# Kernel optimization log

Measured on AMD Instinct MI355X. Metric: run time of the kernel, lower is better.

The kernel has to match this reference:

```python
import jax, jax.numpy as jnp
import numpy as np
from jax import lax

N, C, A, K, D = 2, 256, 3, 20, 256  # batch, channels, anchors, topk person cells, rn_fc_dim
BOX = 4
SIZES = [(80, 128), (40, 64), (20, 32), (10, 16)]
DN = ('NCHW', 'OIHW', 'NCHW')


def _conv(x, w, b):
    return lax.conv_general_dilated(x, w, (1, 1), 'SAME', dimension_numbers=DN) + b[None, :, None, None]


def setup_inputs() -> dict:
    key = jax.random.key(0)
    ks = iter(jax.random.split(key, 40))
    d = {}
    for i, (h, w) in enumerate(SIZES):
        d['feat%d' % i] = jax.random.normal(next(ks), (N, C, h, w), jnp.float32)
    def wfn(shape, s=0.05):
        return jax.random.normal(next(ks), shape, jnp.float32) * s
    d['pc1_w'] = wfn((C, C, 3, 3)); d['pc1_b'] = jnp.zeros((C,), jnp.float32)
    d['pc2_w'] = wfn((C, C, 3, 3)); d['pc2_b'] = jnp.zeros((C,), jnp.float32)
    d['oc1_w'] = wfn((C, C, 3, 3)); d['oc1_b'] = jnp.zeros((C,), jnp.float32)
    d['oc2_w'] = wfn((C, C, 3, 3)); d['oc2_b'] = jnp.zeros((C,), jnp.float32)
    # relation-net FCs: first takes concat(object, person) -> 2C in
    d['rn1_w'] = wfn((D, 2 * C)); d['rn1_b'] = jnp.zeros((D,), jnp.float32)
    d['rn2_w'] = wfn((D, D)); d['rn2_b'] = jnp.zeros((D,), jnp.float32)
    # heads
    d['pl_w'] = wfn((A, C, 1, 1), 0.01); d['pl_b'] = jnp.zeros((A,), jnp.float32)
    d['pd_w'] = wfn((A * BOX, C, 1, 1), 0.01); d['pd_b'] = jnp.zeros((A * BOX,), jnp.float32)
    d['ol_w'] = wfn((A, D), 0.01); d['ol_b'] = jnp.zeros((A,), jnp.float32)
    d['od_w'] = wfn((A * BOX, C, 1, 1), 0.01); d['od_b'] = jnp.zeros((A * BOX,), jnp.float32)
    return d


def _find_top_cells(hidden, logits, topk):
    hid_l, sc_l = [], []
    for h_map, lg in zip(hidden, logits):
        n, c, H, W = h_map.shape
        cell_scores = jnp.max(lg, axis=1).reshape(n, -1)          # (N, HW)
        ts, tc = lax.top_k(cell_scores, topk)                      # (N, K)
        hv = h_map.reshape(n, c, -1)                               # (N, C, HW)
        hid_l.append(jnp.take_along_axis(hv, tc[:, None, :], axis=2))  # (N, C, K)
        sc_l.append(ts)
    scores = jnp.concatenate(sc_l, axis=1)                         # (N, L*K)
    hid = jnp.concatenate(hid_l, axis=2)                           # (N, C, L*K)
    _, keep = lax.top_k(scores, topk)
    return jnp.take_along_axis(hid, keep[:, None, :], axis=2)      # (N, C, K)


def _forward(feats, pc1_w, pc1_b, pc2_w, pc2_b, oc1_w, oc1_b, oc2_w, oc2_b,
             rn1_w, rn1_b, rn2_w, rn2_b, pl_w, pl_b, pd_w, pd_b, ol_w, ol_b, od_w, od_b):
    # person branch
    p_hid, p_log, p_del = [], [], []
    for x in feats:
        x = jax.nn.relu(_conv(x, pc1_w, pc1_b))
        x = jax.nn.relu(_conv(x, pc2_w, pc2_b))
        p_hid.append(x)
        p_log.append(_conv(x, pl_w, pl_b))
        p_del.append(_conv(x, pd_w, pd_b))
    topk_person = _find_top_cells(p_hid, p_log, K)                 # (N, C, K)
    pf = topk_person.transpose(0, 2, 1)                            # (N, K, C)
    # object branch: fc1(concat(o, p)) == o @ Wo.T + p @ Wp.T + b (concat order: object first)
    Wo, Wp = rn1_w[:, :C], rn1_w[:, C:]
    p_proj = jnp.einsum('nkc,dc->nkd', pf, Wp) + rn1_b             # (N, K, D)
    o_log, o_del = [], []
    for x in feats:
        n, _, H, W = x.shape
        y = jax.nn.relu(_conv(x, oc1_w, oc1_b))
        y = jax.nn.relu(_conv(y, oc2_w, oc2_b))
        o_del.append(_conv(y, od_w, od_b))
        yf = y.reshape(n, C, H * W).transpose(0, 2, 1)             # (N, HW, C)
        o_proj = jnp.einsum('nsc,dc->nsd', yf, Wo)                 # (N, HW, D)
        h = jax.nn.relu(o_proj[:, :, None, :] + p_proj[:, None, :, :])  # (N, HW, K, D)
        h = h.sum(axis=2)                                          # (N, HW, D)
        h = jax.nn.relu(jnp.einsum('nsd,ed->nse', h, rn2_w) + rn2_b)
        ol = jnp.einsum('nsd,ad->nsa', h, ol_w) + ol_b             # (N, HW, A)
        o_log.append(ol.transpose(0, 2, 1).reshape(n, A, H, W))
    return tuple(p_log) + tuple(p_del) + tuple(o_log) + tuple(o_del)


def reference(feat0, feat1, feat2, feat3, pc1_w, pc1_b, pc2_w, pc2_b, oc1_w, oc1_b, oc2_w, oc2_b,
              rn1_w, rn1_b, rn2_w, rn2_b, pl_w, pl_b, pd_w, pd_b, ol_w, ol_b, od_w, od_b):
    return _forward([feat0, feat1, feat2, feat3], pc1_w, pc1_b, pc2_w, pc2_b, oc1_w, oc1_b,
                    oc2_w, oc2_b, rn1_w, rn1_b, rn2_w, rn2_b, pl_w, pl_b, pd_w, pd_b,
                    ol_w, ol_b, od_w, od_b)
```

## Files before the change

### kernel.cpp

```cpp
#include <hip/hip_runtime.h>
#include <cstdint>
#include <cstddef>

typedef __bf16 bf16x8 __attribute__((ext_vector_type(8)));
typedef float  f32x16 __attribute__((ext_vector_type(16)));

union U16 { bf16x8 v; uint4 q; };
union U8  { __bf16 h[4]; unsigned long long u; };

typedef __attribute__((address_space(1))) const unsigned char gas_t;
typedef __attribute__((address_space(3))) unsigned char las_t;
__device__ __forceinline__ void async16(const void* g, void* l) {
    __builtin_amdgcn_global_load_lds((gas_t*)g, (las_t*)l, 16, 0, 0);
}

__device__ __forceinline__ int lvl256(int bx) {
    return (bx < 40) ? 0 : (bx < 50) ? 1 : (bx < 53) ? 2 : 3;
}
__device__ __forceinline__ int tbase256(int lv) {
    return (lv == 0) ? 0 : (lv == 1) ? 40 : (lv == 2) ? 50 : 53;
}
__device__ __forceinline__ size_t loffE(int lv) {
    return (lv == 0) ? 0 : (lv == 1) ? 5242880 : (lv == 2) ? 6553600 : 6881280;
}
__device__ __forceinline__ size_t plog_off(int lv) {
    return (lv == 0) ? 0 : (lv == 1) ? 61440 : (lv == 2) ? 76800 : 80640;
}
__device__ __forceinline__ size_t pdel_off(int lv) {
    return (lv == 0) ? 81600 : (lv == 1) ? 327360 : (lv == 2) ? 388800 : 404160;
}
__device__ __forceinline__ size_t olog_off(int lv) {
    return (lv == 0) ? 408000 : (lv == 1) ? 469440 : (lv == 2) ? 484800 : 488640;
}
__device__ __forceinline__ size_t odel_off(int lv) {
    return (lv == 0) ? 489600 : (lv == 1) ? 735360 : (lv == 2) ? 796800 : 812160;
}
__device__ __forceinline__ int soff_l(int lv) {
    return (lv == 0) ? 0 : (lv == 1) ? 20480 : (lv == 2) ? 25600 : 26880;
}

__global__ __launch_bounds__(256) void prep_all_k(
    const float* f0, const float* f1, const float* f2, const float* f3,
    const float* pc1w, const float* pc2w, const float* oc1w, const float* oc2w,
    const float* __restrict__ rn1w, const float* __restrict__ rn2w,
    __bf16* __restrict__ wtap, float* __restrict__ WpT,
    __bf16* __restrict__ Wo16, __bf16* __restrict__ rn216,
    unsigned* __restrict__ zrow32, __bf16* __restrict__ x16)
{
    int bid = blockIdx.x, tid = threadIdx.x;
    if (bid < 576) {
        int which = bid / 144, r = bid - which * 144, t = r >> 4, c16 = r & 15;
        const float* src = (which == 0) ? pc1w : (which == 1) ? pc2w
                         : (which == 2) ? oc1w : oc2w;
        __bf16* dst = wtap + (size_t)which * 589824;
        int co = tid;
        U16 a, b;
#pragma unroll
        for (int j = 0; j < 8; ++j)
            a.v[j] = (__bf16)src[(size_t)(co * 256 + c16 * 16 + j) * 9 + t];
#pragma unroll
        for (int j = 0; j < 8; ++j)
            b.v[j] = (__bf16)src[(size_t)(co * 256 + c16 * 16 + 8 + j) * 9 + t];
        size_t o = ((size_t)((t * 16 + c16) * 256 + co)) << 4;
        *(uint4*)&dst[o] = a.q;
        *(uint4*)&dst[o + 8] = b.q;
    } else if (bid < 832) {
        int d = bid - 576, c = tid;
        WpT[c * 256 + d] = rn1w[(size_t)d * 512 + 256 + c];
        Wo16[((c >> 4) * 256 + d) * 16 + (c & 15)] = (__bf16)rn1w[(size_t)d * 512 + c];
        rn216[((c >> 4) * 256 + d) * 16 + (c & 15)] = (__bf16)rn2w[(size_t)d * 256 + c];
        if (d == 0) zrow32[c] = 0u;
    } else {
        int u = bid - 832;
        int bx = u >> 5, rr = u & 31, n = rr >> 4, ch = rr & 15;
        int lv = lvl256(bx);
        int HW = 10240 >> (2 * lv);
        int p = (bx - tbase256(lv)) * 256 + tid;
        if (p >= HW) return;
        const float* f = (lv == 0) ? f0 : (lv == 1) ? f1 : (lv == 2) ? f2 : f3;
        const float* src = f + (size_t)n * 256 * HW + (size_t)ch * 16 * HW + p;
        U16 a, b;
#pragma unroll
        for (int j = 0; j < 8; ++j) a.v[j] = (__bf16)src[(size_t)j * HW];
#pragma unroll
        for (int j = 0; j < 8; ++j) b.v[j] = (__bf16)src[(size_t)(8 + j) * HW];
        size_t o = loffE(lv) + (size_t)n * HW * 256 + (((size_t)ch * HW + p) << 4);
        *(uint4*)&x16[o] = a.q;
        *(uint4*)&x16[o + 8] = b.q;
    }
}

__global__ __launch_bounds__(256) void conv3x3_v4(
    const __bf16* __restrict__ in16,
    const __bf16* __restrict__ wt0, const __bf16* __restrict__ wt1,
    const float* __restrict__ b0p, const float* __restrict__ b1p,
    const __bf16* __restrict__ zrow,
    __bf16* __restrict__ out0, __bf16* __restrict__ out1)
{
    __shared__ __bf16 Asm[2][9216];

    const int tid = threadIdx.x;
    const int zz = blockIdx.z;
    const int n = zz & 1, br = zz >> 1;
    const __bf16* wt = br ? wt1 : wt0;
    const float* bias = br ? b1p : b0p;
    __bf16* outp = br ? out1 : out0;

    const int bx = blockIdx.x;
    const int lv = lvl256(bx);
    const int lg2W = 7 - lv;
    const int W = 1 << lg2W, H = 80 >> lv;
    const int HW = 10240 >> (2 * lv);
    const size_t ioff = loffE(lv) + (size_t)n * HW * 256;
    const __bf16* inb = in16 + ioff;

    const int tile = bx - tbase256(lv);
    const int sp0 = tile << 8;
    const int npix = min(256, HW - sp0);

    const int w = tid >> 6, l64 = tid & 63;
    const int lane = l64 & 31, half = l64 >> 5;
    const int pix0 = (w << 6) + lane, pix1 = pix0 + 32;
    const int cobase = blockIdx.y << 6;

    int boff0[9], boff1[9];
    {
        const int y0 = sp0 >> lg2W;
        const int py0 = pix0 >> lg2W, px0 = pix0 & (W - 1);
        const int py1 = pix1 >> lg2W, px1 = pix1 & (W - 1);
#pragma unroll
        for (int dy = 0; dy < 3; ++dy)
#pragma unroll
            for (int dx = 0; dx < 3; ++dx) {
                int t = dy * 3 + dx;
                int gy0 = y0 + py0 + dy - 1, gx0 = px0 + dx - 1;
                boff0[t] = ((unsigned)gy0 < (unsigned)H && (unsigned)gx0 < (unsigned)W)
                           ? (((gy0 << lg2W) + gx0) * 32 + half * 16) : -1;
                int gy1 = y0 + py1 + dy - 1, gx1 = px1 + dx - 1;
                boff1[t] = ((unsigned)gy1 < (unsigned)H && (unsigned)gx1 < (unsigned)W)
                           ? (((gy1 << lg2W) + gx1) * 32 + half * 16) : -1;
            }
    }
    const __bf16* zp = zrow + (half << 3);

    const char* wtb = (const char*)wt + cobase * 32;
    auto stage = [&](int c16, int buf) {
        const char* base = wtb + (size_t)c16 * 8192;
        for (int u = w; u < 18; u += 4) {
            int t = u >> 1, hk = u & 1;
            async16(base + (size_t)t * 131072 + hk * 1024 + l64 * 16,
                    &Asm[buf][u * 512]);
        }
    };

    f32x16 acc00 = {}, acc01 = {}, acc10 = {}, acc11 = {};

    stage(0, 0);
    int buf = 0;
    for (int c16 = 0; c16 < 16; ++c16) {
        __syncthreads();
        if (c16 < 15) stage(c16 + 1, buf ^ 1);
        const char* curB = (const char*)inb + (size_t)c16 * HW * 32;
        const __bf16* Ab = &Asm[buf][0];
#pragma unroll
        for (int t = 0; t < 9; ++t) {
            bf16x8 a0 = *(const bf16x8*)&Ab[t * 1024 + lane * 16 + half * 8];
            bf16x8 a1 = *(const bf16x8*)&Ab[t * 1024 + 512 + lane * 16 + half * 8];
            const __bf16* q0 = (boff0[t] >= 0) ? (const __bf16*)(curB + boff0[t]) : zp;
            const __bf16* q1 = (boff1[t] >= 0) ? (const __bf16*)(curB + boff1[t]) : zp;
            bf16x8 b0 = *(const bf16x8*)q0;
            bf16x8 b1 = *(const bf16x8*)q1;
            acc00 = __builtin_amdgcn_mfma_f32_32x32x16_bf16(a0, b0, acc00, 0, 0, 0);
            acc01 = __builtin_amdgcn_mfma_f32_32x32x16_bf16(a0, b1, acc01, 0, 0, 0);
            acc10 = __builtin_amdgcn_mfma_f32_32x32x16_bf16(a1, b0, acc10, 0, 0, 0);
            acc11 = __builtin_amdgcn_mfma_f32_32x32x16_bf16(a1, b1, acc11, 0, 0, 0);
        }
        buf ^= 1;
    }
    const int pixg0 = sp0 + pix0, pixg1 = sp0 + pix1;
    const bool ok0 = (pix0 < npix), ok1 = (pix1 < npix);
#pragma unroll
    for (int b = 0; b < 2; ++b) {
        const f32x16& A0 = b ? acc10 : acc00;
        const f32x16& A1 = b ? acc11 : acc01;
#pragma unroll
        for (int q = 0; q < 4; ++q) {
            int co0 = cobase + b * 32 + q * 8 + half * 4;
            float4 bq = *(const float4*)&bias[co0];
            U8 v0, v1;
            v0.h[0] = (__bf16)fmaxf(A0[q * 4 + 0] + bq.x, 0.f);
            v0.h[1] = (__bf16)fmaxf(A0[q * 4 + 1] + bq.y, 0.f);
            v0.h[2] = (__bf16)fmaxf(A0[q * 4 + 2] + bq.z, 0.f);
            v0.h[3] = (__bf16)fmaxf(A0[q * 4 + 3] + bq.w, 0.f);
            v1.h[0] = (__bf16)fmaxf(A1[q * 4 + 0] + bq.x, 0.f);
            v1.h[1] = (__bf16)fmaxf(A1[q * 4 + 1] + bq.y, 0.f);
            v1.h[2] = (__bf16)fmaxf(A1[q * 4 + 2] + bq.z, 0.f);
            v1.h[3] = (__bf16)fmaxf(A1[q * 4 + 3] + bq.w, 0.f);
            size_t base = ioff + (((size_t)(co0 >> 4) * HW) << 4) + (co0 & 15);
            if (ok0) *(unsigned long long*)&outp[base + ((size_t)pixg0 << 4)] = v0.u;
            if (ok1) *(unsigned long long*)&outp[base + ((size_t)pixg1 << 4)] = v1.u;
        }
    }
}

__global__ __launch_bounds__(256) void heads_k(
    const __bf16* __restrict__ h16p, const __bf16* __restrict__ h16o,
    const float* __restrict__ plw, const float* __restrict__ plb,
    const float* __restrict__ pdw, const float* __restrict__ pdb,
    const float* __restrict__ odw, const float* __restrict__ odb,
    float* __restrict__ out, float* __restrict__ scores)
{
    int bx = blockIdx.x, n = blockIdx.y, br = blockIdx.z;
    int lv = lvl256(bx);
    int HW = 10240 >> (2 * lv);
    int p = (bx - tbase256(lv)) * 256 + threadIdx.x;
    if (p >= HW) return;
    size_t ioff = loffE(lv) + (size_t)n * HW * 256;
    if (br == 0) {
        float acc[15];
#pragma unroll
        for (int a = 0; a < 15; ++a) acc[a] = 0.f;
        for (int ch = 0; ch < 16; ++ch) {
            size_t base = ioff + (((size_t)ch * HW + p) << 4);
            bf16x8 v0 = *(const bf16x8*)&h16p[base];
            bf16x8 v1 = *(const bf16x8*)&h16p[base + 8];
#pragma unroll
            for (int j = 0; j < 16; ++j) {
                float vv = (j < 8) ? (float)v0[j] : (float)v1[j - 8];
                int c = ch * 16 + j;
#pragma unroll
                for (int a = 0; a < 3; ++a)  acc[a]     = fmaf(plw[a * 256 + c], vv, acc[a]);
#pragma unroll
                for (int a = 0; a < 12; ++a) acc[3 + a] = fmaf(pdw[a * 256 + c], vv, acc[3 + a]);
            }
        }
        float sc = -INFINITY;
#pragma unroll
        for (int a = 0; a < 3; ++a) {
            float lg = acc[a] + plb[a];
            out[plog_off(lv) + ((size_t)n * 3 + a) * HW + p] = lg;
            sc = fmaxf(sc, lg);
        }
        scores[soff_l(lv) + (size_t)n * HW + p] = sc;
#pragma unroll
        for (int a = 0; a < 12; ++a)
            out[pdel_off(lv) + ((size_t)n * 12 + a) * HW + p] = acc[3 + a] + pdb[a];
    } else {
        float acc[12];
#pragma unroll
        for (int a = 0; a < 12; ++a) acc[a] = 0.f;
        for (int ch = 0; ch < 16; ++ch) {
            size_t base = ioff + (((size_t)ch * HW + p) << 4);
            bf16x8 v0 = *(const bf16x8*)&h16o[base];
            bf16x8 v1 = *(const bf16x8*)&h16o[base + 8];
#pragma unroll
            for (int j = 0; j < 16; ++j) {
                float vv = (j < 8) ? (float)v0[j] : (float)v1[j - 8];
                int c = ch * 16 + j;
#pragma unroll
                for (int a = 0; a < 12; ++a) acc[a] = fmaf(odw[a * 256 + c], vv, acc[a]);
            }
        }
#pragma unroll
        for (int a = 0; a < 12; ++a)
            out[odel_off(lv) + ((size_t)n * 12 + a) * HW + p] = acc[a] + odb[a];
    }
}

__global__ __launch_bounds__(256) void topk_lvl_k(
    const float* __restrict__ scores, float* __restrict__ lv_sc,
    int* __restrict__ lv_ix)
{
    int l = blockIdx.x, n = blockIdx.y;
    int HW = 10240 >> (2 * l);
    const float* sp = scores + soff_l(l) + (size_t)n * HW;
    int tid = threadIdx.x;
    __shared__ float sc[10240];
    __shared__ float wv4[4];
    __shared__ int wi4[4];
    __shared__ int bcast;
    for (int i = tid; i < HW; i += 256) sc[i] = sp[i];
    __syncthreads();
    float bv = -INFINITY; int bi = 0x7fffffff;
    for (int i = tid; i < HW; i += 256)
        if (sc[i] > bv) { bv = sc[i]; bi = i; }
    const int w = tid >> 6, lane = tid & 63;
    for (int r = 0; r < 20; ++r) {
        float cv = bv; int ci = bi;
#pragma unroll
        for (int off = 32; off > 0; off >>= 1) {
            float ov = __shfl_xor(cv, off);
            int oi = __shfl_xor(ci, off);
            if (ov > cv || (ov == cv && oi < ci)) { cv = ov; ci = oi; }
        }
        if (lane == 0) { wv4[w] = cv; wi4[w] = ci; }
        __syncthreads();
        if (tid == 0) {
            float mv = wv4[0]; int mi = wi4[0];
#pragma unroll
            for (int j = 1; j < 4; ++j)
                if (wv4[j] > mv || (wv4[j] == mv && wi4[j] < mi)) { mv = wv4[j]; mi = wi4[j]; }
            bcast = mi;
            int idx = (n * 4 + l) * 20 + r;
            lv_sc[idx] = mv;
            lv_ix[idx] = mi;
        }
        __syncthreads();
        int mi = bcast;
        if ((mi & 255) == tid) {
            sc[mi] = -INFINITY;
            bv = -INFINITY; bi = 0x7fffffff;
            for (int i = tid; i < HW; i += 256)
                if (sc[i] > bv) { bv = sc[i]; bi = i; }
        }
    }
}

__global__ __launch_bounds__(256) void sel_pproj_k(
    const float* __restrict__ lv_sc, const int* __restrict__ lv_ix,
    const __bf16* __restrict__ h16p, const float* __restrict__ WpT,
    const float* __restrict__ rn1b, float* __restrict__ pp)
{
    int n = blockIdx.x, tid = threadIdx.x;
    __shared__ int selL[20], selC[20];
    __shared__ float pfL[5120];
    __shared__ float wv2[2];
    __shared__ int wi2[2];
    __shared__ int bcast;
    float bv = -INFINITY; int bi = 0x7fffffff;
    if (tid < 80) { bv = lv_sc[n * 80 + tid]; bi = tid; }
    const int w = tid >> 6, lane = tid & 63;
    for (int r = 0; r < 20; ++r) {
        float cv = bv; int ci = bi;
#pragma unroll
        for (int off = 32; off > 0; off >>= 1) {
            float ov = __shfl_xor(cv, off);
            int oi = __shfl_xor(ci, off);
            if (ov > cv || (ov == cv && oi < ci)) { cv = ov; ci = oi; }
        }
        if (lane == 0 && w < 2) { wv2[w] = cv; wi2[w] = ci; }
        __syncthreads();
        if (tid == 0) {
            float mv = wv2[0]; int mi = wi2[0];
            if (wv2[1] > mv || (wv2[1] == mv && wi2[1] < mi)) { mv = wv2[1]; mi = wi2[1]; }
            bcast = mi;
            selL[r] = mi / 20;
            selC[r] = lv_ix[n * 80 + mi];
        }
        __syncthreads();
        if (bcast == bi) bv = -INFINITY;
    }
    for (int t = tid; t < 5120; t += 256) {
        int k = t >> 8, c = t & 255;
        int l = selL[k], cell = selC[k];
        int HW = 10240 >> (2 * l);
        pfL[k * 256 + c] =
            (float)h16p[loffE(l) + (size_t)n * HW * 256 +
                        (((size_t)(c >> 4) * HW + cell) << 4) + (c & 15)];
    }
    __syncthreads();
    float acc[20];
    float bb = rn1b[tid];
#pragma unroll
    for (int k = 0; k < 20; ++k) acc[k] = bb;
    for (int c = 0; c < 256; ++c) {
        float wv = WpT[c * 256 + tid];
#pragma unroll
        for (int k = 0; k < 20; ++k) acc[k] = fmaf(pfL[k * 256 + c], wv, acc[k]);
    }
#pragma unroll
    for (int k = 0; k < 20; ++k)
        pp[(size_t)n * 5120 + k * 256 + tid] = acc[k];
}

__global__ __launch_bounds__(256) void orel_k(
    const __bf16* __restrict__ H16o, const __bf16* __restrict__ Wo16,
    const __bf16* __restrict__ rn216, const float* __restrict__ pp,
    const float* __restrict__ rn2b, const float* __restrict__ olw,
    const float* __restrict__ olb, float* __restrict__ out)
{
    __shared__ __bf16 hb[16 * 64 * 24];
    __shared__ __bf16 pp16[5120];
    const int tid = threadIdx.x;
    const int n = blockIdx.y;
    int bx = blockIdx.x;
    int lv = (bx < 160) ? 0 : (bx < 200) ? 1 : (bx < 210) ? 2 : 3;
    int tb = (lv == 0) ? 0 : (lv == 1) ? 160 : (lv == 2) ? 200 : 210;
    int HW = 10240 >> (2 * lv);
    size_t yoff = loffE(lv) + (size_t)n * HW * 256;
    int p0 = (bx - tb) << 6;
    int npix = min(64, HW - p0);

    {
        const float* ps = pp + (size_t)n * 5120;
        for (int i = tid; i < 1280; i += 256) {
            float4 f = *(const float4*)&ps[i * 4];
            U8 v;
            v.h[0] = (__bf16)f.x; v.h[1] = (__bf16)f.y;
            v.h[2] = (__bf16)f.z; v.h[3] = (__bf16)f.w;
            *(unsigned long long*)&pp16[i * 4] = v.u;
        }
    }
    __syncthreads();

    const int w = tid >> 6, l64 = tid & 63;
    const int lane = l64 & 31, half = l64 >> 5;
    const int dbase = w << 6;

    f32x16 acc00 = {}, acc01 = {}, acc10 = {}, acc11 = {};
    for (int c16 = 0; c16 < 16; ++c16) {
        bf16x8 a0 = *(const bf16x8*)&Wo16[(((c16 << 8) + dbase + lane) << 4) + (half << 3)];
        bf16x8 a1 = *(const bf16x8*)&Wo16[(((c16 << 8) + dbase + 32 + lane) << 4) + (half << 3)];
        bf16x8 b0 = *(const bf16x8*)&H16o[yoff + (((size_t)c16 * HW + p0 + lane) << 4) + (half << 3)];
        bf16x8 b1 = *(const bf16x8*)&H16o[yoff + (((size_t)c16 * HW + p0 + 32 + lane) << 4) + (half << 3)];
        acc00 = __builtin_amdgcn_mfma_f32_32x32x16_bf16(a0, b0, acc00, 0, 0, 0);
        acc01 = __builtin_amdgcn_mfma_f32_32x32x16_bf16(a0, b1, acc01, 0, 0, 0);
        acc10 = __builtin_amdgcn_mfma_f32_32x32x16_bf16(a1, b0, acc10, 0, 0, 0);
        acc11 = __builtin_amdgcn_mfma_f32_32x32x16_bf16(a1, b1, acc11, 0, 0, 0);
    }
#pragma unroll
    for (int b = 0; b < 2; ++b) {
        const f32x16& A0 = b ? acc10 : acc00;
        const f32x16& A1 = b ? acc11 : acc01;
#pragma unroll
        for (int q = 0; q < 4; ++q) {
            int d0 = dbase + b * 32 + q * 8 + half * 4;
            float h0[4] = {0.f, 0.f, 0.f, 0.f}, h1[4] = {0.f, 0.f, 0.f, 0.f};
            for (int k = 0; k < 20; ++k) {
                U8 pk;
                pk.u = *(const unsigned long long*)&pp16[k * 256 + d0];
#pragma unroll
                for (int j = 0; j < 4; ++j) {
                    float pkv = (float)pk.h[j];
                    h0[j] += fmaxf(A0[q * 4 + j] + pkv, 0.f);
                    h1[j] += fmaxf(A1[q * 4 + j] + pkv, 0.f);
                }
            }
            U8 v0, v1;
#pragma unroll
            for (int j = 0; j < 4; ++j) { v0.h[j] = (__bf16)h0[j]; v1.h[j] = (__bf16)h1[j]; }
            *(unsigned long long*)&hb[((d0 >> 4) * 64 + lane) * 24 + (d0 & 15)] = v0.u;
            *(unsigned long long*)&hb[((d0 >> 4) * 64 + 32 + lane) * 24 + (d0 & 15)] = v1.u;
        }
    }
    __syncthreads();
    f32x16 e00 = {}, e01 = {}, e10 = {}, e11 = {};
    for (int d16 = 0; d16 < 16; ++d16) {
        bf16x8 a0 = *(const bf16x8*)&rn216[(((d16 << 8) + dbase + lane) << 4) + (half << 3)];
        bf16x8 a1 = *(const bf16x8*)&rn216[(((d16 << 8) + dbase + 32 + lane) << 4) + (half << 3)];
        bf16x8 b0 = *(const bf16x8*)&hb[(d16 * 64 + lane) * 24 + (half << 3)];
        bf16x8 b1 = *(const bf16x8*)&hb[(d16 * 64 + 32 + lane) * 24 + (half << 3)];
        e00 = __builtin_amdgcn_mfma_f32_32x32x16_bf16(a0, b0, e00, 0, 0, 0);
        e01 = __builtin_amdgcn_mfma_f32_32x32x16_bf16(a0, b1, e01, 0, 0, 0);
        e10 = __builtin_amdgcn_mfma_f32_32x32x16_bf16(a1, b0, e10, 0, 0, 0);
        e11 = __builtin_amdgcn_mfma_f32_32x32x16_bf16(a1, b1, e11, 0, 0, 0);
    }
    __syncthreads();
#pragma unroll
    for (int b = 0; b < 2; ++b) {
        const f32x16& A0 = b ? e10 : e00;
        const f32x16& A1 = b ? e11 : e01;
#pragma unroll
        for (int q = 0; q < 4; ++q) {
            int e0 = dbase + b * 32 + q * 8 + half * 4;
            float4 bb = *(const float4*)&rn2b[e0];
            U8 v0, v1;
            v0.h[0] = (__bf16)fmaxf(A0[q * 4 + 0] + bb.x, 0.f);
            v0.h[1] = (__bf16)fmaxf(A0[q * 4 + 1] + bb.y, 0.f);
            v0.h[2] = (__bf16)fmaxf(A0[q * 4 + 2] + bb.z, 0.f);
            v0.h[3] = (__bf16)fmaxf(A0[q * 4 + 3] + bb.w, 0.f);
            v1.h[0] = (__bf16)fmaxf(A1[q * 4 + 0] + bb.x, 0.f);
            v1.h[1] = (__bf16)fmaxf(A1[q * 4 + 1] + bb.y, 0.f);
            v1.h[2] = (__bf16)fmaxf(A1[q * 4 + 2] + bb.z, 0.f);
            v1.h[3] = (__bf16)fmaxf(A1[q * 4 + 3] + bb.w, 0.f);
            *(unsigned long long*)&hb[((e0 >> 4) * 64 + lane) * 24 + (e0 & 15)] = v0.u;
            *(unsigned long long*)&hb[((e0 >> 4) * 64 + 32 + lane) * 24 + (e0 & 15)] = v1.u;
        }
    }
    __syncthreads();
    if (tid < 192) {
        int px = tid / 3, a = tid - px * 3;
        if (px < npix) {
            float s = olb[a];
            for (int e = 0; e < 256; ++e)
                s = fmaf(olw[a * 256 + e], (float)hb[((e >> 4) * 64 + px) * 24 + (e & 15)], s);
            out[olog_off(lv) + ((size_t)n * 3 + a) * HW + p0 + px] = s;
        }
    }
}

extern "C" void kernel_launch(void* const* d_in, const int* in_sizes, int n_in,
                              void* d_out, int out_size, void* d_ws, size_t ws_size,
                              hipStream_t stream)
{
    const float* feat[4] = {(const float*)d_in[0], (const float*)d_in[1],
                            (const float*)d_in[2], (const float*)d_in[3]};
    const float* pc1w = (const float*)d_in[4];  const float* pc1b = (const float*)d_in[5];
    const float* pc2w = (const float*)d_in[6];  const float* pc2b = (const float*)d_in[7];
    const float* oc1w = (const float*)d_in[8];  const float* oc1b = (const float*)d_in[9];
    const float* oc2w = (const float*)d_in[10]; const float* oc2b = (const float*)d_in[11];
    const float* rn1w = (const float*)d_in[12]; const float* rn1b = (const float*)d_in[13];
    const float* rn2w = (const float*)d_in[14]; const float* rn2b = (const float*)d_in[15];
    const float* plw  = (const float*)d_in[16]; const float* plb  = (const float*)d_in[17];
    const float* pdw  = (const float*)d_in[18]; const float* pdb  = (const float*)d_in[19];
    const float* olw  = (const float*)d_in[20]; const float* olb  = (const float*)d_in[21];
    const float* odw  = (const float*)d_in[22]; const float* odb  = (const float*)d_in[23];

    float* ws = (float*)d_ws;
    __bf16* bufA = (__bf16*)(ws);
    __bf16* bufB = (__bf16*)(ws + 3481600);
    __bf16* bufC = (__bf16*)(ws + 6963200);
    __bf16* wtap = (__bf16*)(ws + 10444800);
    __bf16* wt_pc1 = wtap;
    __bf16* wt_pc2 = wtap + 589824;
    __bf16* wt_oc1 = wtap + 2 * 589824;
    __bf16* wt_oc2 = wtap + 3 * 589824;
    __bf16* Wo16  = (__bf16*)(ws + 11624448);
    __bf16* rn216 = (__bf16*)(ws + 11657216);
    float* WpT    = ws + 11689984;
    float* scores = ws + 11755520;
    float* lv_sc  = ws + 11783040;
    int*   lv_ix  = (int*)(ws + 11783200);
    float* pp     = ws + 11793280;
    __bf16* zrow  = (__bf16*)(ws + 11803520);
    float* out    = (float*)d_out;

    hipLaunchKernelGGL(prep_all_k, dim3(2560), dim3(256), 0, stream,
                       feat[0], feat[1], feat[2], feat[3],
                       pc1w, pc2w, oc1w, oc2w, rn1w, rn2w,
                       wtap, WpT, Wo16, rn216, (unsigned*)zrow, bufA);

    hipLaunchKernelGGL(conv3x3_v4, dim3(54, 4, 4), dim3(256), 0, stream,
                       bufA, wt_pc1, wt_oc1, pc1b, oc1b, zrow, bufB, bufC);
    hipLaunchKernelGGL(conv3x3_v4, dim3(54, 4, 2), dim3(256), 0, stream,
                       bufB, wt_pc2, wt_pc2, pc2b, pc2b, zrow, bufA, bufA);
    hipLaunchKernelGGL(conv3x3_v4, dim3(54, 4, 2), dim3(256), 0, stream,
                       bufC, wt_oc2, wt_oc2, oc2b, oc2b, zrow, bufB, bufB);

    hipLaunchKernelGGL(heads_k, dim3(54, 2, 2), dim3(256), 0, stream,
                       bufA, bufB, plw, plb, pdw, pdb, odw, odb, out, scores);

    hipLaunchKernelGGL(topk_lvl_k, dim3(4, 2), dim3(256), 0, stream,
                       scores, lv_sc, lv_ix);
    hipLaunchKernelGGL(sel_pproj_k, dim3(2), dim3(256), 0, stream,
                       lv_sc, lv_ix, bufA, WpT, rn1b, pp);

    hipLaunchKernelGGL(orel_k, dim3(213, 2), dim3(256), 0, stream,
                       bufB, Wo16, rn216, pp, rn2b, olw, olb, out);
}
```

Baseline: 545.5 us.

## Merge second-layer person/object convs into one launch and re-layout weight tiles

The second 3x3 conv of the person and object towers now runs in a single launch when the workspace is large enough, with separate input pointers per branch and a new output buffer bufD. This removes one kernel launch and lets both branches fill the GPU together. Conv weights are also reordered into a per-64-output-channel, half-split layout so that LDS reads for the A operand are contiguous per lane. The merged path depends on the workspace size check and falls back to two launches otherwise.

Measured after the change: 537.1 us. Within noise of the previous version (-1.5%).

```diff
diff --git a/kernel.cpp b/kernel.cpp
--- a/kernel.cpp
+++ b/kernel.cpp
@@ -53,7 +53,7 @@
         const float* src = (which == 0) ? pc1w : (which == 1) ? pc2w
                          : (which == 2) ? oc1w : oc2w;
         __bf16* dst = wtap + (size_t)which * 589824;
-        int co = tid;
+        int co = tid, cg = co >> 6, co64 = co & 63;
         U16 a, b;
 #pragma unroll
         for (int j = 0; j < 8; ++j)
@@ -61,9 +61,9 @@
 #pragma unroll
         for (int j = 0; j < 8; ++j)
             b.v[j] = (__bf16)src[(size_t)(co * 256 + c16 * 16 + 8 + j) * 9 + t];
-        size_t o = ((size_t)((t * 16 + c16) * 256 + co)) << 4;
-        *(uint4*)&dst[o] = a.q;
-        *(uint4*)&dst[o + 8] = b.q;
+        size_t base = (size_t)t * 65536 + (size_t)c16 * 4096 + (size_t)cg * 1024 + co64 * 8;
+        *(uint4*)&dst[base] = a.q;
+        *(uint4*)&dst[base + 512] = b.q;
     } else if (bid < 832) {
         int d = bid - 576, c = tid;
         WpT[c * 256 + d] = rn1w[(size_t)d * 512 + 256 + c];
@@ -90,21 +90,22 @@
     }
 }
 
-__global__ __launch_bounds__(256) void conv3x3_v4(
-    const __bf16* __restrict__ in16,
-    const __bf16* __restrict__ wt0, const __bf16* __restrict__ wt1,
-    const float* __restrict__ b0p, const float* __restrict__ b1p,
+__global__ __launch_bounds__(256) void conv3x3_v5(
+    const __bf16* __restrict__ inA, const __bf16* __restrict__ inB,
+    const __bf16* __restrict__ wtA, const __bf16* __restrict__ wtB,
+    const float* __restrict__ bA, const float* __restrict__ bB,
     const __bf16* __restrict__ zrow,
-    __bf16* __restrict__ out0, __bf16* __restrict__ out1)
+    __bf16* __restrict__ outA, __bf16* __restrict__ outB)
 {
     __shared__ __bf16 Asm[2][9216];
 
     const int tid = threadIdx.x;
     const int zz = blockIdx.z;
-    const int n = zz & 1, br = zz >> 1;
-    const __bf16* wt = br ? wt1 : wt0;
-    const float* bias = br ? b1p : b0p;
-    __bf16* outp = br ? out1 : out0;
+    const int n = zz & 1, br = (zz >> 1) & 1;
+    const __bf16* in16 = br ? inB : inA;
+    const __bf16* wt = br ? wtB : wtA;
+    const float* bias = br ? bB : bA;
+    __bf16* outp = br ? outB : outA;
 
     const int bx = blockIdx.x;
     const int lv = lvl256(bx);
@@ -143,12 +144,12 @@
     }
     const __bf16* zp = zrow + (half << 3);
 
-    const char* wtb = (const char*)wt + cobase * 32;
+    const char* wtb = (const char*)wt + (blockIdx.y * 2048);
     auto stage = [&](int c16, int buf) {
         const char* base = wtb + (size_t)c16 * 8192;
         for (int u = w; u < 18; u += 4) {
-            int t = u >> 1, hk = u & 1;
-            async16(base + (size_t)t * 131072 + hk * 1024 + l64 * 16,
+            int t = u >> 1, hf = u & 1;
+            async16(base + (size_t)t * 131072 + hf * 1024 + l64 * 16,
                     &Asm[buf][u * 512]);
         }
     };
@@ -164,8 +165,8 @@
         const __bf16* Ab = &Asm[buf][0];
 #pragma unroll
         for (int t = 0; t < 9; ++t) {
-            bf16x8 a0 = *(const bf16x8*)&Ab[t * 1024 + lane * 16 + half * 8];
-            bf16x8 a1 = *(const bf16x8*)&Ab[t * 1024 + 512 + lane * 16 + half * 8];
+            bf16x8 a0 = *(const bf16x8*)&Ab[t * 1024 + half * 512 + lane * 8];
+            bf16x8 a1 = *(const bf16x8*)&Ab[t * 1024 + half * 512 + 256 + lane * 8];
             const __bf16* q0 = (boff0[t] >= 0) ? (const __bf16*)(curB + boff0[t]) : zp;
             const __bf16* q1 = (boff1[t] >= 0) ? (const __bf16*)(curB + boff1[t]) : zp;
             bf16x8 b0 = *(const bf16x8*)q0;
@@ -523,22 +524,34 @@
     int*   lv_ix  = (int*)(ws + 11783200);
     float* pp     = ws + 11793280;
     __bf16* zrow  = (__bf16*)(ws + 11803520);
+    __bf16* bufD  = (__bf16*)(ws + 11803904);
     float* out    = (float*)d_out;
+
+    const bool merged = ws_size >= (size_t)(11803904 + 3481600) * 4;
 
     hipLaunchKernelGGL(prep_all_k, dim3(2560), dim3(256), 0, stream,
                        feat[0], feat[1], feat[2], feat[3],
                        pc1w, pc2w, oc1w, oc2w, rn1w, rn2w,
                        wtap, WpT, Wo16, rn216, (unsigned*)zrow, bufA);
 
-    hipLaunchKernelGGL(conv3x3_v4, dim3(54, 4, 4), dim3(256), 0, stream,
-                       bufA, wt_pc1, wt_oc1, pc1b, oc1b, zrow, bufB, bufC);
-    hipLaunchKernelGGL(conv3x3_v4, dim3(54, 4, 2), dim3(256), 0, stream,
-                       bufB, wt_pc2, wt_pc2, pc2b, pc2b, zrow, bufA, bufA);
-    hipLaunchKernelGGL(conv3x3_v4, dim3(54, 4, 2), dim3(256), 0, stream,
-                       bufC, wt_oc2, wt_oc2, oc2b, oc2b, zrow, bufB, bufB);
+    hipLaunchKernelGGL(conv3x3_v5, dim3(54, 4, 4), dim3(256), 0, stream,
+                       bufA, bufA, wt_pc1, wt_oc1, pc1b, oc1b, zrow, bufB, bufC);
+
+    __bf16* h16o;
+    if (merged) {
+        hipLaunchKernelGGL(conv3x3_v5, dim3(54, 4, 4), dim3(256), 0, stream,
+                           bufB, bufC, wt_pc2, wt_oc2, pc2b, oc2b, zrow, bufA, bufD);
+        h16o = bufD;
+    } else {
+        hipLaunchKernelGGL(conv3x3_v5, dim3(54, 4, 2), dim3(256), 0, stream,
+                           bufB, bufB, wt_pc2, wt_pc2, pc2b, pc2b, zrow, bufA, bufA);
+        hipLaunchKernelGGL(conv3x3_v5, dim3(54, 4, 2), dim3(256), 0, stream,
+                           bufC, bufC, wt_oc2, wt_oc2, oc2b, oc2b, zrow, bufB, bufB);
+        h16o = bufB;
+    }
 
     hipLaunchKernelGGL(heads_k, dim3(54, 2, 2), dim3(256), 0, stream,
-                       bufA, bufB, plw, plb, pdw, pdb, odw, odb, out, scores);
+                       bufA, h16o, plw, plb, pdw, pdb, odw, odb, out, scores);
 
     hipLaunchKernelGGL(topk_lvl_k, dim3(4, 2), dim3(256), 0, stream,
                        scores, lv_sc, lv_ix);
@@ -546,5 +559,5 @@
                        lv_sc, lv_ix, bufA, WpT, rn1b, pp);
 
     hipLaunchKernelGGL(orel_k, dim3(213, 2), dim3(256), 0, stream,
-                       bufB, Wo16, rn216, pp, rn2b, olw, olb, out);
-}
+                       h16o, Wo16, rn216, pp, rn2b, olw, olb, out);
+}
```
